# Kernel tuning notes

Measured on AMD Instinct MI355X. Metric: run time of the kernel, lower is better.

Reference implementation:

```python
import jax, jax.numpy as jnp
import numpy as np

EMA_DECAY = 0.99


def setup_inputs() -> dict:
    key = jax.random.key(0)
    k1, k2, k3 = jax.random.split(key, 3)
    B, T, D, K = 32, 8192, 64, 512
    x = jax.random.normal(k1, (B, T, D), dtype=jnp.float32)
    embedding = jax.random.normal(k2, (K, D), dtype=jnp.float32)
    count = jnp.ones((K,), dtype=jnp.float32)
    sum_embed = jax.random.normal(k3, (K, D), dtype=jnp.float32)
    return {"x": x, "embedding": embedding, "count": count, "sum_embed": sum_embed}


def reference(x, embedding, count, sum_embed):
    # is_training=True path of Quantizer.call
    K, D = embedding.shape
    flat = x.reshape(-1, D)  # [N, D]
    N = flat.shape[0]
    dist = (
        jnp.sum(flat * flat, axis=1, keepdims=True)
        - 2.0 * flat @ embedding.T
        + jnp.sum(embedding * embedding, axis=1)
    )
    encoding_index = jnp.argmin(dist, axis=1)  # [N]

    # one-hot counts and sums expressed as segment sums (avoids [K, N] onehot)
    c = jax.ops.segment_sum(jnp.ones((N,), dtype=jnp.float32), encoding_index, num_segments=K)
    new_sum = jax.ops.segment_sum(flat, encoding_index, num_segments=K)  # [K, D]

    count = count + (1.0 - EMA_DECAY) * (c - count)
    usage = (count >= 1.0).astype(jnp.float32)  # [K]
    count = count * usage + (1.0 - usage)
    sum_embed = sum_embed + (1.0 - EMA_DECAY) * (new_sum - sum_embed)

    # re-seed dead codes with random input vectors
    r = jax.random.randint(jax.random.key(1), (K,), 0, N)
    usage2 = usage[:, None]
    embedding_new = usage2 * (sum_embed / count[:, None]) + (1.0 - usage2) * flat[r]

    quantized = embedding_new[encoding_index].reshape(x.shape)
    # straight-through estimator
    quantized = x + jax.lax.stop_gradient(quantized - x)
    return quantized
```

## Files before the change

### kernel.cpp

```cpp
#include <hip/hip_runtime.h>

#define D 64
#define KC 512
#define EMA_A 0.01f
#define SROWS 1024
#define NCHUNK 256
#define HROWS 1024
#define NHB 256
#define BAND 0.0078125f

typedef float f32x4 __attribute__((ext_vector_type(4)));
typedef float v4f __attribute__((ext_vector_type(4)));
typedef short s8v __attribute__((ext_vector_type(8)));
typedef short s4v __attribute__((ext_vector_type(4)));

__device__ inline unsigned short bf16_rne(float f) {
    unsigned u = __float_as_uint(f);
    return (unsigned short)((u + 0x7fffu + ((u >> 16) & 1u)) >> 16);
}
__device__ inline float bf16_f(unsigned short h) {
    return __uint_as_float(((unsigned)h) << 16);
}

__global__ __launch_bounds__(256) void k_prep(const float* __restrict__ emb,
                                              float* __restrict__ he,
                                              short* __restrict__ gB,
                                              int* __restrict__ wcount) {
    if (blockIdx.x == 0 && threadIdx.x == 0) wcount[0] = 0;
    int k = blockIdx.x * 256 + threadIdx.x;
    if (k >= KC) return;
    int c8 = k >> 6, c = k & 63;
    short* dst = gB + (size_t)c8 * 8192;
    float s = 0.f;
#pragma unroll
    for (int kq = 0; kq < 16; ++kq) {
        float4 v = ((const float4*)(emb + (size_t)k * D))[kq];
        s = fmaf(v.x, v.x, s); s = fmaf(v.y, v.y, s);
        s = fmaf(v.z, v.z, s); s = fmaf(v.w, v.w, s);
        unsigned short h0 = bf16_rne(v.x), h1 = bf16_rne(v.y);
        unsigned short h2 = bf16_rne(v.z), h3 = bf16_rne(v.w);
        s4v hv = {(short)h0, (short)h1, (short)h2, (short)h3};
        s4v lv = {(short)bf16_rne(v.x - bf16_f(h0)),
                  (short)bf16_rne(v.y - bf16_f(h1)),
                  (short)bf16_rne(v.z - bf16_f(h2)),
                  (short)bf16_rne(v.w - bf16_f(h3))};
        int si = c * 64 + (((kq >> 1) ^ (c & 7)) * 8) + (kq & 1) * 4;
        *(s4v*)(&dst[si]) = hv;
        *(s4v*)(&dst[4096 + si]) = lv;
    }
    he[k] = 0.5f * s;
}

__global__ __launch_bounds__(256, 4) void k_assign(
    const float* __restrict__ x, const short* __restrict__ gB,
    const float* __restrict__ he, int* __restrict__ idx,
    int* __restrict__ wlist, int* __restrict__ wcount) {
    __shared__ __align__(16) short LB[2][8192];
    __shared__ int wl_cnt, wl_base;
    __shared__ int wl_rows[128];
    int tid = threadIdx.x;
    int lane = tid & 63, w = tid >> 6, q = lane >> 4, c16 = lane & 15;
    size_t R0 = (size_t)blockIdx.x * 128;
    if (tid == 0) wl_cnt = 0;

    const float4* xg = (const float4*)(x + R0 * D);
#pragma unroll
    for (int p = 0; p < 8; ++p) {
        int flat = p * 256 + tid;
        int row = flat >> 4, kq = flat & 15;
        float4 v = xg[flat];
        unsigned short h0 = bf16_rne(v.x), h1 = bf16_rne(v.y);
        unsigned short h2 = bf16_rne(v.z), h3 = bf16_rne(v.w);
        s4v hv = {(short)h0, (short)h1, (short)h2, (short)h3};
        s4v lv = {(short)bf16_rne(v.x - bf16_f(h0)),
                  (short)bf16_rne(v.y - bf16_f(h1)),
                  (short)bf16_rne(v.z - bf16_f(h2)),
                  (short)bf16_rne(v.w - bf16_f(h3))};
        int si = row * 64 + (((kq >> 1) ^ (row & 7)) * 8) + (kq & 1) * 4;
        *(s4v*)(&LB[0][si]) = hv;
        *(s4v*)(&LB[1][si]) = lv;
    }
    __syncthreads();

    s8v ah[2][2], al[2][2];
#pragma unroll
    for (int rt = 0; rt < 2; ++rt)
#pragma unroll
        for (int ks = 0; ks < 2; ++ks) {
            int row = w * 32 + rt * 16 + c16;
            int kb = (ks * 4 + q) ^ (row & 7);
            ah[rt][ks] = *(const s8v*)(&LB[0][row * 64 + kb * 8]);
            al[rt][ks] = *(const s8v*)(&LB[1][row * 64 + kb * 8]);
        }
    __syncthreads();

#pragma unroll
    for (int p = 0; p < 4; ++p)
        ((int4*)LB[0])[p * 256 + tid] = ((const int4*)gB)[p * 256 + tid];
    __syncthreads();

    float m1[8], m2[8]; int i1[8];
#pragma unroll
    for (int e = 0; e < 8; ++e) { m1[e] = 3.4e38f; m2[e] = 3.4e38f; i1[e] = 0; }

    for (int c8 = 0; c8 < 8; ++c8) {
        if (c8 < 7) {
            const int4* src = (const int4*)(gB + (size_t)(c8 + 1) * 8192);
            int4* dst = (int4*)LB[(c8 + 1) & 1];
#pragma unroll
            for (int p = 0; p < 4; ++p)
                dst[p * 256 + tid] = src[p * 256 + tid];
        }
        const short* LBc = LB[c8 & 1];
#pragma unroll
        for (int ct = 0; ct < 4; ++ct) {
            s8v bh[2], bl[2];
#pragma unroll
            for (int ks = 0; ks < 2; ++ks) {
                int c = ct * 16 + c16;
                int kb = (ks * 4 + q) ^ (c & 7);
                bh[ks] = *(const s8v*)(&LBc[c * 64 + kb * 8]);
                bl[ks] = *(const s8v*)(&LBc[4096 + c * 64 + kb * 8]);
            }
            int cbase = c8 * 64 + ct * 16;
            float hec = he[cbase + c16];
            int ci = cbase + c16;
#pragma unroll
            for (int rt = 0; rt < 2; ++rt) {
                f32x4 acc = {0.f, 0.f, 0.f, 0.f};
                acc = __builtin_amdgcn_mfma_f32_16x16x32_bf16(ah[rt][0], bh[0], acc, 0, 0, 0);
                acc = __builtin_amdgcn_mfma_f32_16x16x32_bf16(ah[rt][1], bh[1], acc, 0, 0, 0);
                acc = __builtin_amdgcn_mfma_f32_16x16x32_bf16(ah[rt][0], bl[0], acc, 0, 0, 0);
                acc = __builtin_amdgcn_mfma_f32_16x16x32_bf16(ah[rt][1], bl[1], acc, 0, 0, 0);
                acc = __builtin_amdgcn_mfma_f32_16x16x32_bf16(al[rt][0], bh[0], acc, 0, 0, 0);
                acc = __builtin_amdgcn_mfma_f32_16x16x32_bf16(al[rt][1], bh[1], acc, 0, 0, 0);
                acc = __builtin_amdgcn_mfma_f32_16x16x32_bf16(al[rt][0], bl[0], acc, 0, 0, 0);
                acc = __builtin_amdgcn_mfma_f32_16x16x32_bf16(al[rt][1], bl[1], acc, 0, 0, 0);
#pragma unroll
                for (int r = 0; r < 4; ++r) {
                    float d = hec - acc[r];
                    int e = rt * 4 + r;
                    m2[e] = fminf(m2[e], fmaxf(d, m1[e]));
                    bool lt = d < m1[e];
                    i1[e] = lt ? ci : i1[e];
                    m1[e] = fminf(m1[e], d);
                }
            }
        }
        __syncthreads();
    }
#pragma unroll
    for (int m = 1; m < 16; m <<= 1) {
#pragma unroll
        for (int e = 0; e < 8; ++e) {
            float om1 = __shfl_xor(m1[e], m);
            float om2 = __shfl_xor(m2[e], m);
            int oi = __shfl_xor(i1[e], m);
            float nm2 = fminf(fminf(m2[e], om2), fmaxf(m1[e], om1));
            bool take = (om1 < m1[e]) || (om1 == m1[e] && oi < i1[e]);
            i1[e] = take ? oi : i1[e];
            m1[e] = fminf(m1[e], om1);
            m2[e] = nm2;
        }
    }
    if (c16 == 0) {
#pragma unroll
        for (int e = 0; e < 8; ++e) {
            int row = (int)R0 + w * 32 + (e >> 2) * 16 + q * 4 + (e & 3);
            idx[row] = i1[e];
            if (m2[e] - m1[e] < BAND) {
                int p = atomicAdd(&wl_cnt, 1);
                wl_rows[p] = row;
            }
        }
    }
    __syncthreads();
    if (tid == 0 && wl_cnt > 0) wl_base = atomicAdd(wcount, wl_cnt);
    __syncthreads();
    for (int i = tid; i < wl_cnt; i += 256) wlist[wl_base + i] = wl_rows[i];
}

__global__ __launch_bounds__(256) void k_recheck(
    const float* __restrict__ x, const float* __restrict__ emb,
    const float* __restrict__ he, const int* __restrict__ wlist,
    const int* __restrict__ wcount, int* __restrict__ idx) {
    int lane = threadIdx.x & 63;
    int wave = (blockIdx.x * 256 + threadIdx.x) >> 6;
    int nwaves = (gridDim.x * 256) >> 6;
    int cnt = wcount[0];
    for (int i = wave; i < cnt; i += nwaves) {
        int row = wlist[i];
        const v4f* xr = (const v4f*)(x + (size_t)row * D);
        v4f X[16];
#pragma unroll
        for (int t = 0; t < 16; ++t) X[t] = xr[t];
        float bd = 3.4e38f; int bi = 0x7fffffff;
#pragma unroll
        for (int j = 0; j < 8; ++j) {
            int c = j * 64 + lane;
            const v4f* er = (const v4f*)(emb + (size_t)c * D);
            v4f s = X[0] * er[0];
#pragma unroll
            for (int t = 1; t < 16; ++t) s += X[t] * er[t];
            float dot = (s.x + s.y) + (s.z + s.w);
            float d = he[c] - dot;
            if (d < bd) { bd = d; bi = c; }
        }
#pragma unroll
        for (int m = 1; m < 64; m <<= 1) {
            float od = __shfl_xor(bd, m);
            int oi = __shfl_xor(bi, m);
            if (od < bd || (od == bd && oi < bi)) { bd = od; bi = oi; }
        }
        if (lane == 0) idx[row] = bi;
    }
}

__global__ __launch_bounds__(256) void k_hist(const int* __restrict__ idx,
                                              float* __restrict__ gcount) {
    __shared__ int hist[KC];
    int tid = threadIdx.x;
    for (int i = tid; i < KC; i += 256) hist[i] = 0;
    __syncthreads();
    int base = blockIdx.x * HROWS;
    for (int r = base + tid; r < base + HROWS; r += 256)
        atomicAdd(&hist[idx[r]], 1);
    __syncthreads();
    for (int i = tid; i < KC; i += 256)
        gcount[(size_t)blockIdx.x * KC + i] = (float)hist[i];
}

__global__ __launch_bounds__(512, 1) void k_segsum(
    const float* __restrict__ x, const int* __restrict__ idx,
    float* __restrict__ gpart) {
    __shared__ int sidx[SROWS];
    __shared__ unsigned xpk[32 * 64];
    int tid = threadIdx.x;
    int lane = tid & 63, w = tid >> 6, q = lane >> 4, c16 = lane & 15;
    int nb0 = blockIdx.x * SROWS;
    for (int i = tid; i < SROWS; i += 512) sidx[i] = idx[nb0 + i];

    f32x4 acc[4][4];
#pragma unroll
    for (int a = 0; a < 4; ++a)
#pragma unroll
        for (int b = 0; b < 4; ++b) acc[a][b] = (f32x4){0.f, 0.f, 0.f, 0.f};

    int row32 = tid >> 4, d4 = tid & 15;
    for (int ch = 0; ch < SROWS / 32; ++ch) {
        __syncthreads();
        float4 v = ((const float4*)(x + (size_t)(nb0 + ch * 32 + row32) * D))[d4];
        float vals[4] = {v.x, v.y, v.z, v.w};
#pragma unroll
        for (int i = 0; i < 4; ++i) {
            unsigned short h = bf16_rne(vals[i]);
            unsigned short l = bf16_rne(vals[i] - bf16_f(h));
            int d = d4 * 4 + i;
            xpk[row32 * 64 + ((d + 2 * row32) & 63)] =
                (unsigned)h | ((unsigned)l << 16);
        }
        __syncthreads();

        int iv[8];
#pragma unroll
        for (int j = 0; j < 8; ++j) iv[j] = sidx[ch * 32 + q * 8 + j];
        s8v af[4];
#pragma unroll
        for (int kt = 0; kt < 4; ++kt) {
            int tgt = w * 64 + kt * 16 + c16;
#pragma unroll
            for (int j = 0; j < 8; ++j)
                af[kt][j] = (iv[j] == tgt) ? (short)0x3F80 : (short)0;
        }
#pragma unroll
        for (int dt = 0; dt < 4; ++dt) {
            s8v bh, bl;
#pragma unroll
            for (int j = 0; j < 8; ++j) {
                int n32 = q * 8 + j;
                unsigned pv = xpk[n32 * 64 + ((dt * 16 + c16 + 2 * n32) & 63)];
                bh[j] = (short)(pv & 0xffff);
                bl[j] = (short)(pv >> 16);
            }
#pragma unroll
            for (int kt = 0; kt < 4; ++kt) {
                acc[kt][dt] = __builtin_amdgcn_mfma_f32_16x16x32_bf16(af[kt], bh, acc[kt][dt], 0, 0, 0);
                acc[kt][dt] = __builtin_amdgcn_mfma_f32_16x16x32_bf16(af[kt], bl, acc[kt][dt], 0, 0, 0);
            }
        }
    }
    float* gp = gpart + (size_t)blockIdx.x * (KC * D);
#pragma unroll
    for (int kt = 0; kt < 4; ++kt)
#pragma unroll
        for (int dt = 0; dt < 4; ++dt)
#pragma unroll
            for (int r = 0; r < 4; ++r) {
                int k = w * 64 + kt * 16 + q * 4 + r;
                gp[k * D + dt * 16 + c16] = acc[kt][dt][r];
            }
}

__global__ __launch_bounds__(256) void k_final(
    const float* __restrict__ gpart, const float* __restrict__ gcount,
    const float* __restrict__ cnt_in, const float* __restrict__ sum_embed,
    float* __restrict__ embnew) {
    __shared__ float cs[4];
    int tid = threadIdx.x;
    int i = blockIdx.x * 256 + tid;
    float s = 0.f;
#pragma unroll 4
    for (int c = 0; c < NCHUNK; ++c) s += gpart[(size_t)c * (KC * D) + i];
    if ((tid & 63) == 0) {
        int k = i >> 6;
        float c = 0.f;
#pragma unroll 4
        for (int b = 0; b < NHB; ++b) c += gcount[(size_t)b * KC + k];
        cs[tid >> 6] = c;
    }
    __syncthreads();
    float c = cs[tid >> 6];
    float c0 = cnt_in[i >> 6];
    float cn = c0 + EMA_A * (c - c0);
    float se0 = sum_embed[i];
    float se = se0 + EMA_A * (s - se0);
    embnew[i] = (cn >= 1.0f) ? (se / cn) : 0.0f;
}

__global__ __launch_bounds__(256) void k_gather(const int* __restrict__ idx,
                                                const float* __restrict__ embnew,
                                                float* __restrict__ out, int N) {
    int g = blockIdx.x * 256 + threadIdx.x;
    int row = g >> 4, q = g & 15;
    if (row >= N) return;
    int k = idx[row];
    const float4* e4 = (const float4*)embnew;
    ((float4*)out)[(size_t)row * (D / 4) + q] = e4[k * (D / 4) + q];
}

extern "C" void kernel_launch(void* const* d_in, const int* in_sizes, int n_in,
                              void* d_out, int out_size, void* d_ws, size_t ws_size,
                              hipStream_t stream) {
    const float* x = (const float*)d_in[0];
    const float* emb = (const float*)d_in[1];
    const float* cnt = (const float*)d_in[2];
    const float* sum_embed = (const float*)d_in[3];
    float* out = (float*)d_out;
    int N = in_sizes[0] / D;

    char* w = (char*)d_ws;
    size_t off = 0;
    int* idx = (int*)(w + off);        off += (size_t)N * 4;
    int* wlist = (int*)(w + off);      off += (size_t)N * 4;
    int* wcount = (int*)(w + off);     off += 16;
    float* he = (float*)(w + off);     off += (size_t)KC * 4;
    short* gB = (short*)(w + off);     off += (size_t)8 * 8192 * 2;
    float* embnew = (float*)(w + off); off += (size_t)KC * D * 4;
    float* gcount = (float*)(w + off); off += (size_t)NHB * KC * 4;
    float* gpart = (float*)(w + off);  off += (size_t)NCHUNK * KC * D * 4;

    k_prep<<<(KC + 255) / 256, 256, 0, stream>>>(emb, he, gB, wcount);
    k_assign<<<N / 128, 256, 0, stream>>>(x, gB, he, idx, wlist, wcount);
    k_recheck<<<512, 256, 0, stream>>>(x, emb, he, wlist, wcount, idx);
    k_hist<<<NHB, 256, 0, stream>>>(idx, gcount);
    k_segsum<<<NCHUNK, 512, 0, stream>>>(x, idx, gpart);
    k_final<<<(KC * D) / 256, 256, 0, stream>>>(gpart, gcount, cnt, sum_embed, embnew);
    k_gather<<<((size_t)N * (D / 4)) / 256, 256, 0, stream>>>(idx, embnew, out, N);
}
```

Baseline: 321.1 us.

## Restructure assign to 512 threads, fuse histogram into segsum, rework final reduction

k_assign now runs 512 threads, each wave handling 16 rows, with one single-buffered codebook chunk in shared memory. The hi and lo input halves are staged one after the other, which shrinks LDS use and allows higher occupancy, but drops the prefetch double-buffering. The histogram kernel is folded into k_segsum, which also processes 64 rows per staging step. k_final is rewritten to use one block per code with split reductions over chunks, and one kernel launch is removed.

```diff
diff --git a/kernel.cpp b/kernel.cpp
--- a/kernel.cpp
+++ b/kernel.cpp
@@ -5,8 +5,6 @@
 #define EMA_A 0.01f
 #define SROWS 1024
 #define NCHUNK 256
-#define HROWS 1024
-#define NHB 256
 #define BAND 0.0078125f
 
 typedef float f32x4 __attribute__((ext_vector_type(4)));
@@ -51,11 +49,11 @@
     he[k] = 0.5f * s;
 }
 
-__global__ __launch_bounds__(256, 4) void k_assign(
+__global__ __launch_bounds__(512, 6) void k_assign(
     const float* __restrict__ x, const short* __restrict__ gB,
     const float* __restrict__ he, int* __restrict__ idx,
     int* __restrict__ wlist, int* __restrict__ wcount) {
-    __shared__ __align__(16) short LB[2][8192];
+    __shared__ __align__(16) short LB[8192];
     __shared__ int wl_cnt, wl_base;
     __shared__ int wl_rows[128];
     int tid = threadIdx.x;
@@ -64,54 +62,60 @@
     if (tid == 0) wl_cnt = 0;
 
     const float4* xg = (const float4*)(x + R0 * D);
-#pragma unroll
-    for (int p = 0; p < 8; ++p) {
-        int flat = p * 256 + tid;
+    s4v lo_keep[4];
+#pragma unroll
+    for (int p = 0; p < 4; ++p) {
+        int flat = p * 512 + tid;
         int row = flat >> 4, kq = flat & 15;
         float4 v = xg[flat];
         unsigned short h0 = bf16_rne(v.x), h1 = bf16_rne(v.y);
         unsigned short h2 = bf16_rne(v.z), h3 = bf16_rne(v.w);
         s4v hv = {(short)h0, (short)h1, (short)h2, (short)h3};
-        s4v lv = {(short)bf16_rne(v.x - bf16_f(h0)),
-                  (short)bf16_rne(v.y - bf16_f(h1)),
-                  (short)bf16_rne(v.z - bf16_f(h2)),
-                  (short)bf16_rne(v.w - bf16_f(h3))};
+        lo_keep[p] = (s4v){(short)bf16_rne(v.x - bf16_f(h0)),
+                           (short)bf16_rne(v.y - bf16_f(h1)),
+                           (short)bf16_rne(v.z - bf16_f(h2)),
+                           (short)bf16_rne(v.w - bf16_f(h3))};
         int si = row * 64 + (((kq >> 1) ^ (row & 7)) * 8) + (kq & 1) * 4;
-        *(s4v*)(&LB[0][si]) = hv;
-        *(s4v*)(&LB[1][si]) = lv;
-    }
-    __syncthreads();
-
-    s8v ah[2][2], al[2][2];
-#pragma unroll
-    for (int rt = 0; rt < 2; ++rt)
+        *(s4v*)(&LB[si]) = hv;
+    }
+    __syncthreads();
+    s8v ah[2], al[2];
+    {
+        int row = w * 16 + c16;
 #pragma unroll
         for (int ks = 0; ks < 2; ++ks) {
-            int row = w * 32 + rt * 16 + c16;
             int kb = (ks * 4 + q) ^ (row & 7);
-            ah[rt][ks] = *(const s8v*)(&LB[0][row * 64 + kb * 8]);
-            al[rt][ks] = *(const s8v*)(&LB[1][row * 64 + kb * 8]);
-        }
-    __syncthreads();
-
-#pragma unroll
-    for (int p = 0; p < 4; ++p)
-        ((int4*)LB[0])[p * 256 + tid] = ((const int4*)gB)[p * 256 + tid];
-    __syncthreads();
-
-    float m1[8], m2[8]; int i1[8];
-#pragma unroll
-    for (int e = 0; e < 8; ++e) { m1[e] = 3.4e38f; m2[e] = 3.4e38f; i1[e] = 0; }
+            ah[ks] = *(const s8v*)(&LB[row * 64 + kb * 8]);
+        }
+    }
+    __syncthreads();
+#pragma unroll
+    for (int p = 0; p < 4; ++p) {
+        int flat = p * 512 + tid;
+        int row = flat >> 4, kq = flat & 15;
+        int si = row * 64 + (((kq >> 1) ^ (row & 7)) * 8) + (kq & 1) * 4;
+        *(s4v*)(&LB[si]) = lo_keep[p];
+    }
+    __syncthreads();
+    {
+        int row = w * 16 + c16;
+#pragma unroll
+        for (int ks = 0; ks < 2; ++ks) {
+            int kb = (ks * 4 + q) ^ (row & 7);
+            al[ks] = *(const s8v*)(&LB[row * 64 + kb * 8]);
+        }
+    }
+
+    float m1[4], m2[4]; int i1[4];
+#pragma unroll
+    for (int e = 0; e < 4; ++e) { m1[e] = 3.4e38f; m2[e] = 3.4e38f; i1[e] = 0; }
 
     for (int c8 = 0; c8 < 8; ++c8) {
-        if (c8 < 7) {
-            const int4* src = (const int4*)(gB + (size_t)(c8 + 1) * 8192);
-            int4* dst = (int4*)LB[(c8 + 1) & 1];
-#pragma unroll
-            for (int p = 0; p < 4; ++p)
-                dst[p * 256 + tid] = src[p * 256 + tid];
-        }
-        const short* LBc = LB[c8 & 1];
+        __syncthreads();
+        const int4* src = (const int4*)(gB + (size_t)c8 * 8192);
+        ((int4*)LB)[tid] = src[tid];
+        ((int4*)LB)[512 + tid] = src[512 + tid];
+        __syncthreads();
 #pragma unroll
         for (int ct = 0; ct < 4; ++ct) {
             s8v bh[2], bl[2];
@@ -119,40 +123,35 @@
             for (int ks = 0; ks < 2; ++ks) {
                 int c = ct * 16 + c16;
                 int kb = (ks * 4 + q) ^ (c & 7);
-                bh[ks] = *(const s8v*)(&LBc[c * 64 + kb * 8]);
-                bl[ks] = *(const s8v*)(&LBc[4096 + c * 64 + kb * 8]);
+                bh[ks] = *(const s8v*)(&LB[c * 64 + kb * 8]);
+                bl[ks] = *(const s8v*)(&LB[4096 + c * 64 + kb * 8]);
             }
             int cbase = c8 * 64 + ct * 16;
             float hec = he[cbase + c16];
             int ci = cbase + c16;
-#pragma unroll
-            for (int rt = 0; rt < 2; ++rt) {
-                f32x4 acc = {0.f, 0.f, 0.f, 0.f};
-                acc = __builtin_amdgcn_mfma_f32_16x16x32_bf16(ah[rt][0], bh[0], acc, 0, 0, 0);
-                acc = __builtin_amdgcn_mfma_f32_16x16x32_bf16(ah[rt][1], bh[1], acc, 0, 0, 0);
-                acc = __builtin_amdgcn_mfma_f32_16x16x32_bf16(ah[rt][0], bl[0], acc, 0, 0, 0);
-                acc = __builtin_amdgcn_mfma_f32_16x16x32_bf16(ah[rt][1], bl[1], acc, 0, 0, 0);
-                acc = __builtin_amdgcn_mfma_f32_16x16x32_bf16(al[rt][0], bh[0], acc, 0, 0, 0);
-                acc = __builtin_amdgcn_mfma_f32_16x16x32_bf16(al[rt][1], bh[1], acc, 0, 0, 0);
-                acc = __builtin_amdgcn_mfma_f32_16x16x32_bf16(al[rt][0], bl[0], acc, 0, 0, 0);
-                acc = __builtin_amdgcn_mfma_f32_16x16x32_bf16(al[rt][1], bl[1], acc, 0, 0, 0);
-#pragma unroll
-                for (int r = 0; r < 4; ++r) {
-                    float d = hec - acc[r];
-                    int e = rt * 4 + r;
-                    m2[e] = fminf(m2[e], fmaxf(d, m1[e]));
-                    bool lt = d < m1[e];
-                    i1[e] = lt ? ci : i1[e];
-                    m1[e] = fminf(m1[e], d);
-                }
-            }
-        }
-        __syncthreads();
+            f32x4 a0 = {0.f, 0.f, 0.f, 0.f}, a1 = {0.f, 0.f, 0.f, 0.f};
+            a0 = __builtin_amdgcn_mfma_f32_16x16x32_bf16(ah[0], bh[0], a0, 0, 0, 0);
+            a0 = __builtin_amdgcn_mfma_f32_16x16x32_bf16(ah[1], bh[1], a0, 0, 0, 0);
+            a0 = __builtin_amdgcn_mfma_f32_16x16x32_bf16(ah[0], bl[0], a0, 0, 0, 0);
+            a0 = __builtin_amdgcn_mfma_f32_16x16x32_bf16(ah[1], bl[1], a0, 0, 0, 0);
+            a1 = __builtin_amdgcn_mfma_f32_16x16x32_bf16(al[0], bh[0], a1, 0, 0, 0);
+            a1 = __builtin_amdgcn_mfma_f32_16x16x32_bf16(al[1], bh[1], a1, 0, 0, 0);
+            a1 = __builtin_amdgcn_mfma_f32_16x16x32_bf16(al[0], bl[0], a1, 0, 0, 0);
+            a1 = __builtin_amdgcn_mfma_f32_16x16x32_bf16(al[1], bl[1], a1, 0, 0, 0);
+#pragma unroll
+            for (int r = 0; r < 4; ++r) {
+                float d = (hec - a0[r]) - a1[r];
+                m2[r] = fminf(m2[r], fmaxf(d, m1[r]));
+                bool lt = d < m1[r];
+                i1[r] = lt ? ci : i1[r];
+                m1[r] = fminf(m1[r], d);
+            }
+        }
     }
 #pragma unroll
     for (int m = 1; m < 16; m <<= 1) {
 #pragma unroll
-        for (int e = 0; e < 8; ++e) {
+        for (int e = 0; e < 4; ++e) {
             float om1 = __shfl_xor(m1[e], m);
             float om2 = __shfl_xor(m2[e], m);
             int oi = __shfl_xor(i1[e], m);
@@ -165,8 +164,8 @@
     }
     if (c16 == 0) {
 #pragma unroll
-        for (int e = 0; e < 8; ++e) {
-            int row = (int)R0 + w * 32 + (e >> 2) * 16 + q * 4 + (e & 3);
+        for (int e = 0; e < 4; ++e) {
+            int row = (int)R0 + w * 16 + q * 4 + e;
             idx[row] = i1[e];
             if (m2[e] - m1[e] < BAND) {
                 int p = atomicAdd(&wl_cnt, 1);
@@ -177,7 +176,7 @@
     __syncthreads();
     if (tid == 0 && wl_cnt > 0) wl_base = atomicAdd(wcount, wl_cnt);
     __syncthreads();
-    for (int i = tid; i < wl_cnt; i += 256) wlist[wl_base + i] = wl_rows[i];
+    for (int i = tid; i < wl_cnt; i += 512) wlist[wl_base + i] = wl_rows[i];
 }
 
 __global__ __launch_bounds__(256) void k_recheck(
@@ -216,29 +215,19 @@
     }
 }
 
-__global__ __launch_bounds__(256) void k_hist(const int* __restrict__ idx,
-                                              float* __restrict__ gcount) {
-    __shared__ int hist[KC];
-    int tid = threadIdx.x;
-    for (int i = tid; i < KC; i += 256) hist[i] = 0;
-    __syncthreads();
-    int base = blockIdx.x * HROWS;
-    for (int r = base + tid; r < base + HROWS; r += 256)
-        atomicAdd(&hist[idx[r]], 1);
-    __syncthreads();
-    for (int i = tid; i < KC; i += 256)
-        gcount[(size_t)blockIdx.x * KC + i] = (float)hist[i];
-}
-
 __global__ __launch_bounds__(512, 1) void k_segsum(
     const float* __restrict__ x, const int* __restrict__ idx,
-    float* __restrict__ gpart) {
+    float* __restrict__ gpart, float* __restrict__ gcount) {
     __shared__ int sidx[SROWS];
-    __shared__ unsigned xpk[32 * 64];
+    __shared__ unsigned xpk[64 * 64];
+    __shared__ int hist[KC];
     int tid = threadIdx.x;
     int lane = tid & 63, w = tid >> 6, q = lane >> 4, c16 = lane & 15;
     int nb0 = blockIdx.x * SROWS;
     for (int i = tid; i < SROWS; i += 512) sidx[i] = idx[nb0 + i];
+    hist[tid] = 0;
+    __syncthreads();
+    for (int i = tid; i < SROWS; i += 512) atomicAdd(&hist[sidx[i]], 1);
 
     f32x4 acc[4][4];
 #pragma unroll
@@ -246,46 +235,53 @@
 #pragma unroll
         for (int b = 0; b < 4; ++b) acc[a][b] = (f32x4){0.f, 0.f, 0.f, 0.f};
 
-    int row32 = tid >> 4, d4 = tid & 15;
-    for (int ch = 0; ch < SROWS / 32; ++ch) {
+    for (int ch = 0; ch < SROWS / 64; ++ch) {
         __syncthreads();
-        float4 v = ((const float4*)(x + (size_t)(nb0 + ch * 32 + row32) * D))[d4];
-        float vals[4] = {v.x, v.y, v.z, v.w};
-#pragma unroll
-        for (int i = 0; i < 4; ++i) {
-            unsigned short h = bf16_rne(vals[i]);
-            unsigned short l = bf16_rne(vals[i] - bf16_f(h));
-            int d = d4 * 4 + i;
-            xpk[row32 * 64 + ((d + 2 * row32) & 63)] =
-                (unsigned)h | ((unsigned)l << 16);
+#pragma unroll
+        for (int pp = 0; pp < 2; ++pp) {
+            int flat = pp * 512 + tid;
+            int r64 = flat >> 4, d4 = flat & 15;
+            float4 v = ((const float4*)(x + (size_t)(nb0 + ch * 64 + r64) * D))[d4];
+            float vals[4] = {v.x, v.y, v.z, v.w};
+#pragma unroll
+            for (int i = 0; i < 4; ++i) {
+                unsigned short h = bf16_rne(vals[i]);
+                unsigned short l = bf16_rne(vals[i] - bf16_f(h));
+                int d = d4 * 4 + i;
+                xpk[r64 * 64 + ((d + 2 * r64) & 63)] =
+                    (unsigned)h | ((unsigned)l << 16);
+            }
         }
         __syncthreads();
-
-        int iv[8];
-#pragma unroll
-        for (int j = 0; j < 8; ++j) iv[j] = sidx[ch * 32 + q * 8 + j];
-        s8v af[4];
-#pragma unroll
-        for (int kt = 0; kt < 4; ++kt) {
-            int tgt = w * 64 + kt * 16 + c16;
+#pragma unroll
+        for (int s = 0; s < 2; ++s) {
+            int iv[8];
 #pragma unroll
             for (int j = 0; j < 8; ++j)
-                af[kt][j] = (iv[j] == tgt) ? (short)0x3F80 : (short)0;
-        }
-#pragma unroll
-        for (int dt = 0; dt < 4; ++dt) {
-            s8v bh, bl;
-#pragma unroll
-            for (int j = 0; j < 8; ++j) {
-                int n32 = q * 8 + j;
-                unsigned pv = xpk[n32 * 64 + ((dt * 16 + c16 + 2 * n32) & 63)];
-                bh[j] = (short)(pv & 0xffff);
-                bl[j] = (short)(pv >> 16);
-            }
+                iv[j] = sidx[ch * 64 + s * 32 + q * 8 + j];
+            s8v af[4];
 #pragma unroll
             for (int kt = 0; kt < 4; ++kt) {
-                acc[kt][dt] = __builtin_amdgcn_mfma_f32_16x16x32_bf16(af[kt], bh, acc[kt][dt], 0, 0, 0);
-                acc[kt][dt] = __builtin_amdgcn_mfma_f32_16x16x32_bf16(af[kt], bl, acc[kt][dt], 0, 0, 0);
+                int tgt = w * 64 + kt * 16 + c16;
+#pragma unroll
+                for (int j = 0; j < 8; ++j)
+                    af[kt][j] = (iv[j] == tgt) ? (short)0x3F80 : (short)0;
+            }
+#pragma unroll
+            for (int dt = 0; dt < 4; ++dt) {
+                s8v bh, bl;
+#pragma unroll
+                for (int j = 0; j < 8; ++j) {
+                    int n = s * 32 + q * 8 + j;
+                    unsigned pv = xpk[n * 64 + ((dt * 16 + c16 + 2 * n) & 63)];
+                    bh[j] = (short)(pv & 0xffff);
+                    bl[j] = (short)(pv >> 16);
+                }
+#pragma unroll
+                for (int kt = 0; kt < 4; ++kt) {
+                    acc[kt][dt] = __builtin_amdgcn_mfma_f32_16x16x32_bf16(af[kt], bh, acc[kt][dt], 0, 0, 0);
+                    acc[kt][dt] = __builtin_amdgcn_mfma_f32_16x16x32_bf16(af[kt], bl, acc[kt][dt], 0, 0, 0);
+                }
             }
         }
     }
@@ -299,32 +295,36 @@
                 int k = w * 64 + kt * 16 + q * 4 + r;
                 gp[k * D + dt * 16 + c16] = acc[kt][dt][r];
             }
+    __syncthreads();
+    gcount[(size_t)blockIdx.x * KC + tid] = (float)hist[tid];
 }
 
 __global__ __launch_bounds__(256) void k_final(
     const float* __restrict__ gpart, const float* __restrict__ gcount,
     const float* __restrict__ cnt_in, const float* __restrict__ sum_embed,
     float* __restrict__ embnew) {
-    __shared__ float cs[4];
+    __shared__ float sp[4][64];
+    __shared__ float cp[256];
+    int k = blockIdx.x;
     int tid = threadIdx.x;
-    int i = blockIdx.x * 256 + tid;
+    int d = tid & 63, g = tid >> 6;
     float s = 0.f;
-#pragma unroll 4
-    for (int c = 0; c < NCHUNK; ++c) s += gpart[(size_t)c * (KC * D) + i];
-    if ((tid & 63) == 0) {
-        int k = i >> 6;
-        float c = 0.f;
-#pragma unroll 4
-        for (int b = 0; b < NHB; ++b) c += gcount[(size_t)b * KC + k];
-        cs[tid >> 6] = c;
-    }
-    __syncthreads();
-    float c = cs[tid >> 6];
-    float c0 = cnt_in[i >> 6];
-    float cn = c0 + EMA_A * (c - c0);
-    float se0 = sum_embed[i];
-    float se = se0 + EMA_A * (s - se0);
-    embnew[i] = (cn >= 1.0f) ? (se / cn) : 0.0f;
+    for (int c = g * 64; c < g * 64 + 64; ++c)
+        s += gpart[(size_t)c * (KC * D) + k * D + d];
+    sp[g][d] = s;
+    cp[tid] = gcount[(size_t)tid * KC + k];
+    __syncthreads();
+    if (g == 0) {
+        float st = sp[0][d] + sp[1][d] + sp[2][d] + sp[3][d];
+        float cv = cp[4 * d] + cp[4 * d + 1] + cp[4 * d + 2] + cp[4 * d + 3];
+#pragma unroll
+        for (int m = 1; m < 64; m <<= 1) cv += __shfl_xor(cv, m);
+        float c0 = cnt_in[k];
+        float cn = c0 + EMA_A * (cv - c0);
+        float se0 = sum_embed[k * D + d];
+        float se = se0 + EMA_A * (st - se0);
+        embnew[k * D + d] = (cn >= 1.0f) ? (se / cn) : 0.0f;
+    }
 }
 
 __global__ __launch_bounds__(256) void k_gather(const int* __restrict__ idx,
@@ -356,14 +356,13 @@
     float* he = (float*)(w + off);     off += (size_t)KC * 4;
     short* gB = (short*)(w + off);     off += (size_t)8 * 8192 * 2;
     float* embnew = (float*)(w + off); off += (size_t)KC * D * 4;
-    float* gcount = (float*)(w + off); off += (size_t)NHB * KC * 4;
+    float* gcount = (float*)(w + off); off += (size_t)NCHUNK * KC * 4;
     float* gpart = (float*)(w + off);  off += (size_t)NCHUNK * KC * D * 4;
 
     k_prep<<<(KC + 255) / 256, 256, 0, stream>>>(emb, he, gB, wcount);
-    k_assign<<<N / 128, 256, 0, stream>>>(x, gB, he, idx, wlist, wcount);
+    k_assign<<<N / 128, 512, 0, stream>>>(x, gB, he, idx, wlist, wcount);
     k_recheck<<<512, 256, 0, stream>>>(x, emb, he, wlist, wcount, idx);
-    k_hist<<<NHB, 256, 0, stream>>>(idx, gcount);
-    k_segsum<<<NCHUNK, 512, 0, stream>>>(x, idx, gpart);
-    k_final<<<(KC * D) / 256, 256, 0, stream>>>(gpart, gcount, cnt, sum_embed, embnew);
+    k_segsum<<<NCHUNK, 512, 0, stream>>>(x, idx, gpart, gcount);
+    k_final<<<KC, 256, 0, stream>>>(gpart, gcount, cnt, sum_embed, embnew);
     k_gather<<<((size_t)N * (D / 4)) / 256, 256, 0, stream>>>(idx, embnew, out, N);
 }
```

Result: faster. 313.8 us (-2.3%).
